# Performance work log

Measured on AMD Instinct MI355X. Metric: run time of the kernel, lower is better.

Reference implementation:

```python
import jax, jax.numpy as jnp
import numpy as np

B, T, C = 4, 2048, 768
H, D = 12, 64          # num heads, head size
MLP = 3072
EPS = 1e-6
SCALE = C ** (-0.5)    # NOTE: source scales by n_embd**-0.5, not head_size**-0.5


def setup_inputs() -> dict:
    key = jax.random.key(0)
    ks = jax.random.split(key, 12)
    s = 0.02
    return {
        "x":     jax.random.normal(ks[0], (B, T, C), jnp.float32),
        "Wq":    jax.random.normal(ks[1], (H, C, D), jnp.float32) * s,
        "Wk":    jax.random.normal(ks[2], (H, C, D), jnp.float32) * s,
        "Wv":    jax.random.normal(ks[3], (H, C, D), jnp.float32) * s,
        "Wo":    jax.random.normal(ks[4], (H * D, C), jnp.float32) * s,
        "bo":    jnp.zeros((C,), jnp.float32),
        "ln1_g": jnp.ones((C,), jnp.float32),
        "ln1_b": jnp.zeros((C,), jnp.float32),
        "ln2_g": jnp.ones((C,), jnp.float32),
        "ln2_b": jnp.zeros((C,), jnp.float32),
        "W1":    jax.random.normal(ks[5], (C, MLP), jnp.float32) * s,
        "b1":    jnp.zeros((MLP,), jnp.float32),
        "W2":    jax.random.normal(ks[6], (MLP, C), jnp.float32) * s,
        "b2":    jnp.zeros((C,), jnp.float32),
    }


def _ln(x, g, b):
    mu = jnp.mean(x, axis=-1, keepdims=True)
    var = jnp.var(x, axis=-1, keepdims=True)
    return (x - mu) * jax.lax.rsqrt(var + EPS) * g + b


def reference(x, Wq, Wk, Wv, Wo, bo, ln1_g, ln1_b, ln2_g, ln2_b, W1, b1, W2, b2):
    xn = _ln(x, ln1_g, ln1_b)
    # batched per-head projections: [B,T,C] x [H,C,D] -> [B,H,T,D]
    q = jnp.einsum("btc,hcd->bhtd", xn, Wq)
    k = jnp.einsum("btc,hcd->bhtd", xn, Wk)
    v = jnp.einsum("btc,hcd->bhtd", xn, Wv)
    wei = jnp.einsum("bhtd,bhsd->bhts", q, k) * SCALE  # [B,H,T,T]
    wei = jax.nn.softmax(wei, axis=-1)
    attn = jnp.einsum("bhts,bhsd->bhtd", wei, v)
    # concat heads along feature dim (head order preserved)
    attn = attn.transpose(0, 2, 1, 3).reshape(B, T, H * D)
    sa = attn @ Wo + bo
    x2 = sa + x                      # residual 1 (dropout = identity in eval)
    y = _ln(x2, ln2_g, ln2_b)
    y = jax.nn.gelu(y @ W1 + b1, approximate=False) @ W2 + b2
    return x2 + y                    # residual 2
```

## Files before the change

kernel.cpp:

```cpp
#include <hip/hip_runtime.h>
#include <hip/hip_bf16.h>
#include <cstdint>
#include <cmath>

#define B_ 4
#define T_ 2048
#define C_ 768
#define H_ 12
#define D_ 64
#define MLP_ 3072
#define BT_ (B_*T_)

typedef __hip_bfloat16 hbf;
typedef __bf16 bf16_t;
typedef bf16_t bf16x8 __attribute__((ext_vector_type(8)));
typedef bf16_t bf16x4 __attribute__((ext_vector_type(4)));
typedef float f32x4 __attribute__((ext_vector_type(4)));

static __device__ __forceinline__ void load_lds16(const void* g, void* l) {
    __builtin_amdgcn_global_load_lds(
        (const __attribute__((address_space(1))) unsigned int*)g,
        (__attribute__((address_space(3))) unsigned int*)l, 16, 0, 0);
}

__global__ __launch_bounds__(256) void transpose_pack(
    const float* __restrict__ src, hbf* __restrict__ dst, int R, int S)
{
    __shared__ float tl[64 * 65];
    src += (size_t)blockIdx.z * R * S;
    dst += (size_t)blockIdx.z * R * S;
    const int r0 = blockIdx.y * 64, s0 = blockIdx.x * 64;
    const int c = threadIdx.x & 63, q = threadIdx.x >> 6;
#pragma unroll
    for (int j = 0; j < 16; ++j) {
        int r = q + j * 4;
        tl[r * 65 + c] = src[(size_t)(r0 + r) * S + s0 + c];
    }
    __syncthreads();
#pragma unroll
    for (int j = 0; j < 16; ++j) {
        int s = q + j * 4;
        dst[(size_t)(s0 + s) * R + r0 + c] = __float2bfloat16(tl[c * 65 + s]);
    }
}

__global__ __launch_bounds__(256) void ln_kernel(
    const float* __restrict__ x, const float* __restrict__ g,
    const float* __restrict__ bb, hbf* __restrict__ out)
{
    __shared__ float red[8];
    const int row = blockIdx.x;
    const float* xr = x + (size_t)row * C_;
    const int t = threadIdx.x;
    float v0 = xr[t], v1 = xr[t + 256], v2 = xr[t + 512];
    float s = v0 + v1 + v2;
    float s2 = v0 * v0 + v1 * v1 + v2 * v2;
#pragma unroll
    for (int m = 1; m < 64; m <<= 1) {
        s  += __shfl_xor(s,  m, 64);
        s2 += __shfl_xor(s2, m, 64);
    }
    if ((t & 63) == 0) { red[t >> 6] = s; red[4 + (t >> 6)] = s2; }
    __syncthreads();
    float S  = red[0] + red[1] + red[2] + red[3];
    float S2 = red[4] + red[5] + red[6] + red[7];
    float mu  = S * (1.0f / C_);
    float var = S2 * (1.0f / C_) - mu * mu;
    float inv = rsqrtf(var + 1e-6f);
    hbf* orow = out + (size_t)row * C_;
    orow[t]       = __float2bfloat16((v0 - mu) * inv * g[t]       + bb[t]);
    orow[t + 256] = __float2bfloat16((v1 - mu) * inv * g[t + 256] + bb[t + 256]);
    orow[t + 512] = __float2bfloat16((v2 - mu) * inv * g[t + 512] + bb[t + 512]);
}

template<int EPI>
__global__ __launch_bounds__(256, 2) void gemm_kernel(
    const hbf* __restrict__ A, const hbf* __restrict__ Bt,
    float* __restrict__ outF, hbf* __restrict__ outH,
    const float* __restrict__ bias, const float* __restrict__ resid,
    int M, int N, int K,
    hbf* __restrict__ qb, hbf* __restrict__ kb,
    float scale, int gx)
{
    __shared__ hbf sA0[128 * 64], sA1[128 * 64];
    __shared__ hbf sB0[128 * 64], sB1[128 * 64];
    const int tid = threadIdx.x;
    const int lane = tid & 63;
    const int wid = tid >> 6;
    const int wm = wid >> 1, wn = wid & 1;
    const int lr = lane & 15, hg = lane >> 4;
    const int bid = blockIdx.x, nwg = gridDim.x;
    const int wg = (bid & 7) * (nwg >> 3) + (bid >> 3);
    const int bx = wg % gx, by = wg / gx;
    const int row0 = by * 128;
    const int col0 = bx * 128;

    f32x4 acc[4][4] = {};

    int offG[4];
    const int Kb = K * 2;
#pragma unroll
    for (int i = 0; i < 4; ++i) {
        int c = tid + i * 256;
        offG[i] = (c >> 3) * Kb + (((c & 7) ^ ((c >> 3) & 7)) << 4);
    }
    const char* gA = (const char*)(A + (size_t)row0 * K);
    const char* gB = (const char*)(Bt + (size_t)col0 * K);

    auto stage = [&](int kt, hbf* sAd, hbf* sBd) {
        const int kb2 = kt * 128;
#pragma unroll
        for (int i = 0; i < 4; ++i) {
            load_lds16(gA + (size_t)(offG[i] + kb2), (char*)sAd + i * 4096 + wid * 1024);
            load_lds16(gB + (size_t)(offG[i] + kb2), (char*)sBd + i * 4096 + wid * 1024);
        }
    };
    auto compute = [&](const hbf* sAc, const hbf* sBc) {
#pragma unroll
        for (int kf = 0; kf < 2; ++kf) {
            const int sl = ((kf * 4 + hg) ^ (lr & 7)) << 4;
            bf16x8 af[4], bfr[4];
#pragma unroll
            for (int m = 0; m < 4; ++m)
                af[m] = *(const bf16x8*)((const char*)sAc + (wm * 64 + m * 16 + lr) * 128 + sl);
#pragma unroll
            for (int n = 0; n < 4; ++n)
                bfr[n] = *(const bf16x8*)((const char*)sBc + (wn * 64 + n * 16 + lr) * 128 + sl);
#pragma unroll
            for (int m = 0; m < 4; ++m)
#pragma unroll
                for (int n = 0; n < 4; ++n)
                    acc[m][n] = __builtin_amdgcn_mfma_f32_16x16x32_bf16(af[m], bfr[n], acc[m][n], 0, 0, 0);
        }
    };

    const int NK = K >> 6;
    stage(0, sA0, sB0);
    __syncthreads();
    for (int kt = 0; kt < NK; kt += 2) {
        stage(kt + 1, sA1, sB1);
        compute(sA0, sB0);
        __syncthreads();
        if (kt + 2 < NK) stage(kt + 2, sA0, sB0);
        compute(sA1, sB1);
        __syncthreads();
    }

#pragma unroll
    for (int m = 0; m < 4; ++m) {
#pragma unroll
        for (int n = 0; n < 4; ++n) {
#pragma unroll
            for (int j = 0; j < 4; ++j) {
                int row = row0 + wm * 64 + m * 16 + hg * 4 + j;
                int col = col0 + wn * 64 + n * 16 + lr;
                float v = acc[m][n][j];
                if constexpr (EPI == 0) {
                    outH[(size_t)row * N + col] = __float2bfloat16(v);
                } else if constexpr (EPI == 1) {
                    outF[(size_t)row * N + col] = v + bias[col] + resid[(size_t)row * N + col];
                } else if constexpr (EPI == 2) {
                    float tt = v + bias[col];
                    float ge = 0.5f * tt * (1.0f + erff(tt * 0.70710678118654752f));
                    outH[(size_t)row * N + col] = __float2bfloat16(ge);
                } else {
                    int typ = col / C_;
                    int rr = col - typ * C_;
                    int h = rr >> 6, d = rr & 63;
                    int b = row >> 11, t = row & (T_ - 1);
                    size_t bh = (size_t)b * H_ + h;
                    if (typ == 0) qb[(bh * T_ + t) * D_ + d] = __float2bfloat16(v * scale);
                    else          kb[(bh * T_ + t) * D_ + d] = __float2bfloat16(v);
                }
            }
        }
    }
}

__global__ __launch_bounds__(256, 3) void attn_kernel(
    const hbf* __restrict__ qg, const hbf* __restrict__ kg,
    const hbf* __restrict__ vg, hbf* __restrict__ outA)
{
    __shared__ hbf sK0[64 * 64], sK1[64 * 64];
    __shared__ hbf sV0[64 * 64], sV1[64 * 64];
    __shared__ hbf sP[4 * 32 * 64];
    const int tid = threadIdx.x, lane = tid & 63, wid = tid >> 6;
    const int lr = lane & 15, hg = lane >> 4;
    const int wg = (blockIdx.x & 7) * 96 + (blockIdx.x >> 3);
    const int bh = wg >> 4;
    const int b = bh / H_, h = bh - b * H_;
    const int wr0 = (wg & 15) * 128 + wid * 32;
    const hbf* qbh = qg + (size_t)bh * T_ * D_;
    const hbf* kbh = kg + (size_t)bh * T_ * D_;
    const hbf* vbh = vg + (size_t)h * 64 * BT_ + (size_t)b * T_;

    bf16x8 a_q[2][2];
#pragma unroll
    for (int m = 0; m < 2; ++m)
#pragma unroll
        for (int kf = 0; kf < 2; ++kf)
            a_q[m][kf] = *(const bf16x8*)(qbh + (size_t)(wr0 + m * 16 + lr) * D_ + kf * 32 + hg * 8);

    f32x4 o[2][4] = {};
    float mreg[2] = {-3e38f, -3e38f};
    float lrun[2] = {0.0f, 0.0f};

    int offK[2], offV[2];
#pragma unroll
    for (int i = 0; i < 2; ++i) {
        int c = tid + i * 256;
        int sw = ((c & 7) ^ ((c >> 3) & 7)) << 4;
        offK[i] = (c >> 3) * 128 + sw;
        offV[i] = (c >> 3) * (BT_ * 2) + sw;
    }
    hbf* sPw = sP + wid * (32 * 64);
    const int sl0 = ((0 * 4 + hg) ^ (lr & 7)) << 4;
    const int sl1 = ((1 * 4 + hg) ^ (lr & 7)) << 4;
    const int bcast = hg * 20;

    auto stage = [&](int itn, hbf* sKd, hbf* sVd) {
        const char* kp = (const char*)kbh + (size_t)itn * 8192;
        const char* vp = (const char*)vbh + (size_t)itn * 128;
#pragma unroll
        for (int i = 0; i < 2; ++i) {
            load_lds16(kp + offK[i], (char*)sKd + i * 4096 + wid * 1024);
            load_lds16(vp + offV[i], (char*)sVd + i * 4096 + wid * 1024);
        }
    };

    auto tile = [&](const hbf* sKc, const hbf* sVc) {
        f32x4 st[4][2] = {};
        __builtin_amdgcn_s_setprio(1);
#pragma unroll
        for (int kf = 0; kf < 2; ++kf) {
            const int sl = kf ? sl1 : sl0;
#pragma unroll
            for (int n = 0; n < 4; ++n) {
                bf16x8 ak = *(const bf16x8*)((const char*)sKc + (n * 16 + lr) * 128 + sl);
                st[n][0] = __builtin_amdgcn_mfma_f32_16x16x32_bf16(ak, a_q[0][kf], st[n][0], 0, 0, 0);
                st[n][1] = __builtin_amdgcn_mfma_f32_16x16x32_bf16(ak, a_q[1][kf], st[n][1], 0, 0, 0);
            }
        }
        __builtin_amdgcn_s_setprio(0);

#pragma unroll
        for (int m = 0; m < 2; ++m) {
            float t = st[0][m][0];
#pragma unroll
            for (int n = 0; n < 4; ++n)
#pragma unroll
                for (int j = 0; j < 4; ++j)
                    if (n + j > 0) t = fmaxf(t, st[n][m][j]);
            t = fmaxf(t, __shfl_xor(t, 16, 64));
            t = fmaxf(t, __shfl_xor(t, 32, 64));
            if (__any(t - mreg[m] > 8.0f)) {
                float nm = fmaxf(mreg[m], t);
                float fac = __expf(mreg[m] - nm);
                mreg[m] = nm;
                lrun[m] *= fac;
                float fb[4];
#pragma unroll
                for (int j = 0; j < 4; ++j)
                    fb[j] = __shfl(fac, bcast + j, 64);
#pragma unroll
                for (int nd = 0; nd < 4; ++nd)
#pragma unroll
                    for (int j = 0; j < 4; ++j)
                        o[m][nd][j] *= fb[j];
            }
            float ps = 0.0f;
            const int r = m * 16 + lr;
#pragma unroll
            for (int n = 0; n < 4; ++n) {
                float p0 = __expf(st[n][m][0] - mreg[m]);
                float p1 = __expf(st[n][m][1] - mreg[m]);
                float p2 = __expf(st[n][m][2] - mreg[m]);
                float p3 = __expf(st[n][m][3] - mreg[m]);
                ps += (p0 + p1) + (p2 + p3);
                bf16x4 w;
                w[0] = (bf16_t)p0; w[1] = (bf16_t)p1; w[2] = (bf16_t)p2; w[3] = (bf16_t)p3;
                *(bf16x4*)((char*)sPw + r * 128 +
                           (((n * 2 + (hg >> 1)) ^ (r & 7)) << 4) + ((hg & 1) * 8)) = w;
            }
            ps += __shfl_xor(ps, 16, 64);
            ps += __shfl_xor(ps, 32, 64);
            lrun[m] += ps;
        }

        __builtin_amdgcn_s_setprio(1);
#pragma unroll
        for (int kf = 0; kf < 2; ++kf) {
            const int sl = kf ? sl1 : sl0;
            bf16x8 ap0 = *(const bf16x8*)((const char*)sPw + lr * 128 + sl);
            bf16x8 ap1 = *(const bf16x8*)((const char*)sPw + (16 + lr) * 128 + sl);
#pragma unroll
            for (int nd = 0; nd < 4; ++nd) {
                bf16x8 bv = *(const bf16x8*)((const char*)sVc + (nd * 16 + lr) * 128 + sl);
                o[0][nd] = __builtin_amdgcn_mfma_f32_16x16x32_bf16(ap0, bv, o[0][nd], 0, 0, 0);
                o[1][nd] = __builtin_amdgcn_mfma_f32_16x16x32_bf16(ap1, bv, o[1][nd], 0, 0, 0);
            }
        }
        __builtin_amdgcn_s_setprio(0);
    };

    const int NT = T_ / 64;
    stage(0, sK0, sV0);
    __syncthreads();
    for (int it = 0; it < NT; it += 2) {
        stage(it + 1, sK1, sV1);
        tile(sK0, sV0);
        __syncthreads();
        if (it + 2 < NT) stage(it + 2, sK0, sV0);
        tile(sK1, sV1);
        __syncthreads();
    }

    float lb[2][4];
#pragma unroll
    for (int m = 0; m < 2; ++m)
#pragma unroll
        for (int j = 0; j < 4; ++j)
            lb[m][j] = __shfl(lrun[m], bcast + j, 64);
#pragma unroll
    for (int m = 0; m < 2; ++m)
#pragma unroll
        for (int nd = 0; nd < 4; ++nd)
#pragma unroll
            for (int j = 0; j < 4; ++j) {
                int row = wr0 + m * 16 + hg * 4 + j;
                int col = nd * 16 + lr;
                float val = o[m][nd][j] / lb[m][j];
                outA[((size_t)(b * T_ + row)) * C_ + h * D_ + col] = __float2bfloat16(val);
            }
}

extern "C" void kernel_launch(void* const* d_in, const int* in_sizes, int n_in,
                              void* d_out, int out_size, void* d_ws, size_t ws_size,
                              hipStream_t stream)
{
    const float* x    = (const float*)d_in[0];
    const float* Wq   = (const float*)d_in[1];
    const float* Wk   = (const float*)d_in[2];
    const float* Wv   = (const float*)d_in[3];
    const float* Wo   = (const float*)d_in[4];
    const float* bo   = (const float*)d_in[5];
    const float* ln1g = (const float*)d_in[6];
    const float* ln1b = (const float*)d_in[7];
    const float* ln2g = (const float*)d_in[8];
    const float* ln2b = (const float*)d_in[9];
    const float* W1   = (const float*)d_in[10];
    const float* b1   = (const float*)d_in[11];
    const float* W2   = (const float*)d_in[12];
    const float* b2   = (const float*)d_in[13];
    float* out = (float*)d_out;
    char* ws = (char*)d_ws;

    hbf*  xn    = (hbf*)(ws + 0);
    hbf*  WqkT  = (hbf*)(ws + 12582912);
    hbf*  WvT   = (hbf*)(ws + 14942208);
    hbf*  qb    = (hbf*)(ws + 16121856);
    hbf*  kb    = (hbf*)(ws + 28704768);
    hbf*  vT    = (hbf*)(ws + 41287680);
    hbf*  h1    = (hbf*)(ws + 0);
    hbf*  attnB = (hbf*)(ws + 53870592);
    hbf*  yln   = (hbf*)(ws + 53870592);
    float* x2   = (float*)(ws + 66453504);
    hbf*  WoT   = (hbf*)(ws + 91619328);
    hbf*  W1T   = (hbf*)(ws + 92798976);
    hbf*  W2T   = (hbf*)(ws + 97517568);

    const float SCALE = 0.036084391824351615f;

    transpose_pack<<<dim3(1, 12, 12), 256, 0, stream>>>(Wq, WqkT, 768, 64);
    transpose_pack<<<dim3(1, 12, 12), 256, 0, stream>>>(Wk, WqkT + 768 * 768, 768, 64);
    transpose_pack<<<dim3(1, 12, 12), 256, 0, stream>>>(Wv, WvT, 768, 64);
    transpose_pack<<<dim3(12, 12, 1), 256, 0, stream>>>(Wo, WoT, 768, 768);
    transpose_pack<<<dim3(48, 12, 1), 256, 0, stream>>>(W1, W1T, 768, 3072);
    transpose_pack<<<dim3(12, 48, 1), 256, 0, stream>>>(W2, W2T, 3072, 768);
    ln_kernel<<<8192, 256, 0, stream>>>(x, ln1g, ln1b, xn);
    gemm_kernel<3><<<768, 256, 0, stream>>>(xn, WqkT, nullptr, nullptr, nullptr, nullptr,
        8192, 1536, 768, qb, kb, SCALE, 12);
    gemm_kernel<0><<<384, 256, 0, stream>>>(WvT, xn, nullptr, vT, nullptr, nullptr,
        768, BT_, 768, nullptr, nullptr, 1.0f, 64);
    attn_kernel<<<768, 256, 0, stream>>>(qb, kb, vT, attnB);
    gemm_kernel<1><<<384, 256, 0, stream>>>(attnB, WoT, x2, nullptr, bo, x,
        8192, 768, 768, nullptr, nullptr, 1.0f, 6);
    ln_kernel<<<8192, 256, 0, stream>>>(x2, ln2g, ln2b, yln);
    gemm_kernel<2><<<1536, 256, 0, stream>>>(yln, W1T, nullptr, h1, b1, nullptr,
        8192, 3072, 768, nullptr, nullptr, 1.0f, 24);
    gemm_kernel<1><<<384, 256, 0, stream>>>(h1, W2T, out, nullptr, b2, x2,
        8192, 768, 3072, nullptr, nullptr, 1.0f, 6);
}
```

Measured before the change: 303.2 us.

## Single-buffer GEMM LDS, add 128x64 tile variant, fuse QKV weight packing

The GEMM drops LDS double buffering and now issues the next tile's global-to-LDS load only after compute finishes, behind a barrier. This shrinks shared memory so occupancy can rise to 3 blocks per CU. A TN=64 tile variant gives the two N=768 projection GEMMs 768 blocks instead of 384, for better CU fill. The three Q/K/V weight transpose launches are merged into one kernel. The risk is losing load/compute overlap inside each block, which then has to be hidden by running more blocks at once.

```diff
diff --git a/kernel.cpp b/kernel.cpp
--- a/kernel.cpp
+++ b/kernel.cpp
@@ -41,6 +41,31 @@
     for (int j = 0; j < 16; ++j) {
         int s = q + j * 4;
         dst[(size_t)(s0 + s) * R + r0 + c] = __float2bfloat16(tl[c * 65 + s]);
+    }
+}
+
+__global__ __launch_bounds__(256) void pack_qkv3(
+    const float* __restrict__ Wq, const float* __restrict__ Wk,
+    const float* __restrict__ Wv, hbf* __restrict__ WqkT, hbf* __restrict__ WvT)
+{
+    __shared__ float tl[64 * 65];
+    const int z = blockIdx.z;
+    const int mtx = z / 12, head = z - mtx * 12;
+    const float* src = (mtx == 0 ? Wq : mtx == 1 ? Wk : Wv) + (size_t)head * 49152;
+    hbf* dst = (mtx == 2) ? (WvT + (size_t)head * 49152)
+                          : (WqkT + (size_t)(mtx * 12 + head) * 49152);
+    const int r0 = blockIdx.y * 64;
+    const int c = threadIdx.x & 63, q = threadIdx.x >> 6;
+#pragma unroll
+    for (int j = 0; j < 16; ++j) {
+        int r = q + j * 4;
+        tl[r * 65 + c] = src[(size_t)(r0 + r) * 64 + c];
+    }
+    __syncthreads();
+#pragma unroll
+    for (int j = 0; j < 16; ++j) {
+        int s = q + j * 4;
+        dst[(size_t)s * 768 + r0 + c] = __float2bfloat16(tl[c * 65 + s]);
     }
 }
 
@@ -73,8 +98,8 @@
     orow[t + 512] = __float2bfloat16((v2 - mu) * inv * g[t + 512] + bb[t + 512]);
 }
 
-template<int EPI>
-__global__ __launch_bounds__(256, 2) void gemm_kernel(
+template<int EPI, int TN>
+__global__ __launch_bounds__(256, 3) void gemm_kernel(
     const hbf* __restrict__ A, const hbf* __restrict__ Bt,
     float* __restrict__ outF, hbf* __restrict__ outH,
     const float* __restrict__ bias, const float* __restrict__ resid,
@@ -82,20 +107,23 @@
     hbf* __restrict__ qb, hbf* __restrict__ kb,
     float scale, int gx)
 {
-    __shared__ hbf sA0[128 * 64], sA1[128 * 64];
-    __shared__ hbf sB0[128 * 64], sB1[128 * 64];
+    constexpr int AM = (TN == 128) ? 4 : 2;
+    constexpr int NB_B = (TN == 128) ? 4 : 2;
+    __shared__ hbf sA[128 * 64];
+    __shared__ hbf sB[TN * 64];
     const int tid = threadIdx.x;
     const int lane = tid & 63;
     const int wid = tid >> 6;
-    const int wm = wid >> 1, wn = wid & 1;
     const int lr = lane & 15, hg = lane >> 4;
     const int bid = blockIdx.x, nwg = gridDim.x;
     const int wg = (bid & 7) * (nwg >> 3) + (bid >> 3);
     const int bx = wg % gx, by = wg / gx;
     const int row0 = by * 128;
-    const int col0 = bx * 128;
-
-    f32x4 acc[4][4] = {};
+    const int col0 = bx * TN;
+    const int wrow = (TN == 128) ? (wid >> 1) * 64 : wid * 32;
+    const int wcol = (TN == 128) ? (wid & 1) * 64 : 0;
+
+    f32x4 acc[AM][4] = {};
 
     int offG[4];
     const int Kb = K * 2;
@@ -107,53 +135,48 @@
     const char* gA = (const char*)(A + (size_t)row0 * K);
     const char* gB = (const char*)(Bt + (size_t)col0 * K);
 
-    auto stage = [&](int kt, hbf* sAd, hbf* sBd) {
+    auto stage = [&](int kt) {
         const int kb2 = kt * 128;
 #pragma unroll
-        for (int i = 0; i < 4; ++i) {
-            load_lds16(gA + (size_t)(offG[i] + kb2), (char*)sAd + i * 4096 + wid * 1024);
-            load_lds16(gB + (size_t)(offG[i] + kb2), (char*)sBd + i * 4096 + wid * 1024);
-        }
+        for (int i = 0; i < 4; ++i)
+            load_lds16(gA + (size_t)(offG[i] + kb2), (char*)sA + i * 4096 + wid * 1024);
+#pragma unroll
+        for (int i = 0; i < NB_B; ++i)
+            load_lds16(gB + (size_t)(offG[i] + kb2), (char*)sB + i * 4096 + wid * 1024);
     };
-    auto compute = [&](const hbf* sAc, const hbf* sBc) {
+
+    const int NK = K >> 6;
+    stage(0);
+    for (int kt = 0; kt < NK; ++kt) {
+        __syncthreads();
 #pragma unroll
         for (int kf = 0; kf < 2; ++kf) {
             const int sl = ((kf * 4 + hg) ^ (lr & 7)) << 4;
-            bf16x8 af[4], bfr[4];
-#pragma unroll
-            for (int m = 0; m < 4; ++m)
-                af[m] = *(const bf16x8*)((const char*)sAc + (wm * 64 + m * 16 + lr) * 128 + sl);
+            bf16x8 af[AM], bfr[4];
+#pragma unroll
+            for (int m = 0; m < AM; ++m)
+                af[m] = *(const bf16x8*)((const char*)sA + (wrow + m * 16 + lr) * 128 + sl);
 #pragma unroll
             for (int n = 0; n < 4; ++n)
-                bfr[n] = *(const bf16x8*)((const char*)sBc + (wn * 64 + n * 16 + lr) * 128 + sl);
-#pragma unroll
-            for (int m = 0; m < 4; ++m)
+                bfr[n] = *(const bf16x8*)((const char*)sB + (wcol + n * 16 + lr) * 128 + sl);
+#pragma unroll
+            for (int m = 0; m < AM; ++m)
 #pragma unroll
                 for (int n = 0; n < 4; ++n)
                     acc[m][n] = __builtin_amdgcn_mfma_f32_16x16x32_bf16(af[m], bfr[n], acc[m][n], 0, 0, 0);
         }
-    };
-
-    const int NK = K >> 6;
-    stage(0, sA0, sB0);
-    __syncthreads();
-    for (int kt = 0; kt < NK; kt += 2) {
-        stage(kt + 1, sA1, sB1);
-        compute(sA0, sB0);
         __syncthreads();
-        if (kt + 2 < NK) stage(kt + 2, sA0, sB0);
-        compute(sA1, sB1);
-        __syncthreads();
-    }
-
-#pragma unroll
-    for (int m = 0; m < 4; ++m) {
+        if (kt + 1 < NK) stage(kt + 1);
+    }
+
+#pragma unroll
+    for (int m = 0; m < AM; ++m) {
 #pragma unroll
         for (int n = 0; n < 4; ++n) {
 #pragma unroll
             for (int j = 0; j < 4; ++j) {
-                int row = row0 + wm * 64 + m * 16 + hg * 4 + j;
-                int col = col0 + wn * 64 + n * 16 + lr;
+                int row = row0 + wrow + m * 16 + hg * 4 + j;
+                int col = col0 + wcol + n * 16 + lr;
                 float v = acc[m][n][j];
                 if constexpr (EPI == 0) {
                     outH[(size_t)row * N + col] = __float2bfloat16(v);
@@ -371,23 +394,21 @@
 
     const float SCALE = 0.036084391824351615f;
 
-    transpose_pack<<<dim3(1, 12, 12), 256, 0, stream>>>(Wq, WqkT, 768, 64);
-    transpose_pack<<<dim3(1, 12, 12), 256, 0, stream>>>(Wk, WqkT + 768 * 768, 768, 64);
-    transpose_pack<<<dim3(1, 12, 12), 256, 0, stream>>>(Wv, WvT, 768, 64);
+    pack_qkv3<<<dim3(1, 12, 36), 256, 0, stream>>>(Wq, Wk, Wv, WqkT, WvT);
     transpose_pack<<<dim3(12, 12, 1), 256, 0, stream>>>(Wo, WoT, 768, 768);
     transpose_pack<<<dim3(48, 12, 1), 256, 0, stream>>>(W1, W1T, 768, 3072);
     transpose_pack<<<dim3(12, 48, 1), 256, 0, stream>>>(W2, W2T, 3072, 768);
     ln_kernel<<<8192, 256, 0, stream>>>(x, ln1g, ln1b, xn);
-    gemm_kernel<3><<<768, 256, 0, stream>>>(xn, WqkT, nullptr, nullptr, nullptr, nullptr,
+    gemm_kernel<3,128><<<768, 256, 0, stream>>>(xn, WqkT, nullptr, nullptr, nullptr, nullptr,
         8192, 1536, 768, qb, kb, SCALE, 12);
-    gemm_kernel<0><<<384, 256, 0, stream>>>(WvT, xn, nullptr, vT, nullptr, nullptr,
+    gemm_kernel<0,128><<<384, 256, 0, stream>>>(WvT, xn, nullptr, vT, nullptr, nullptr,
         768, BT_, 768, nullptr, nullptr, 1.0f, 64);
     attn_kernel<<<768, 256, 0, stream>>>(qb, kb, vT, attnB);
-    gemm_kernel<1><<<384, 256, 0, stream>>>(attnB, WoT, x2, nullptr, bo, x,
-        8192, 768, 768, nullptr, nullptr, 1.0f, 6);
+    gemm_kernel<1,64><<<768, 256, 0, stream>>>(attnB, WoT, x2, nullptr, bo, x,
+        8192, 768, 768, nullptr, nullptr, 1.0f, 12);
     ln_kernel<<<8192, 256, 0, stream>>>(x2, ln2g, ln2b, yln);
-    gemm_kernel<2><<<1536, 256, 0, stream>>>(yln, W1T, nullptr, h1, b1, nullptr,
+    gemm_kernel<2,128><<<1536, 256, 0, stream>>>(yln, W1T, nullptr, h1, b1, nullptr,
         8192, 3072, 768, nullptr, nullptr, 1.0f, 24);
-    gemm_kernel<1><<<384, 256, 0, stream>>>(h1, W2T, out, nullptr, b2, x2,
-        8192, 768, 3072, nullptr, nullptr, 1.0f, 6);
-}
+    gemm_kernel<1,64><<<768, 256, 0, stream>>>(h1, W2T, out, nullptr, b2, x2,
+        8192, 768, 3072, nullptr, nullptr, 1.0f, 12);
+}
```

After: 289.5 us. 1.05x faster.
